# Performance work log

Measured on AMD Instinct MI355X. Metric: run time of the kernel, lower is better.

The kernel has to match this reference:

```python
import jax, jax.numpy as jnp
import numpy as np

B, S, H = 1, 2048, 1024          # batch, seq, hidden_size
INTER, K, DST, DTR = 2048, 4, 16, 64  # intermediate, kernel, ssm_state, dt_rank


def setup_inputs() -> dict:
    key = jax.random.key(0)
    ks = jax.random.split(key, 10)
    sc = 0.02
    return {
        "x": jax.random.normal(ks[0], (B, S, H), jnp.float32),
        "W_in": jax.random.normal(ks[1], (H, 2 * INTER), jnp.float32) * sc,
        "conv_w": jax.random.normal(ks[2], (K, 1, INTER), jnp.float32) * sc,
        "conv_b": jax.random.normal(ks[3], (INTER,), jnp.float32) * sc,
        "W_x": jax.random.normal(ks[4], (INTER, DTR + 2 * DST), jnp.float32) * sc,
        "W_dt": jax.random.normal(ks[5], (DTR, INTER), jnp.float32) * sc,
        "b_dt": jax.random.normal(ks[6], (INTER,), jnp.float32) * sc,
        "A_log": jax.random.normal(ks[7], (INTER, DST), jnp.float32) * sc,
        "D": jax.random.normal(ks[8], (INTER,), jnp.float32) * sc,
        "W_out": jax.random.normal(ks[9], (INTER, H), jnp.float32) * sc,
    }


def _ssm(dA, dBu, C):
    # dA, dBu: (b, s, h, d); C: (b, s, d) -> y: (b, s, h)
    xs = (jnp.moveaxis(dA, 1, 0), jnp.moveaxis(dBu, 1, 0), jnp.moveaxis(C, 1, 0))
    state0 = jnp.zeros(dA.shape[:1] + dA.shape[2:], dA.dtype)  # (b, h, d)

    def step(state, inp):
        Ai, dBui, Ci = inp  # (b,h,d), (b,h,d), (b,d)
        state = Ai * state + dBui
        y = jnp.einsum('bhd,bd->bh', state, Ci)
        return state, y

    _, ys = jax.lax.scan(step, state0, xs)  # ys: (s, b, h)
    return jnp.moveaxis(ys, 0, 1)


def reference(x, W_in, conv_w, conv_b, W_x, W_dt, b_dt, A_log, D, W_out):
    proj = x @ W_in                              # (b, s, 2*inter)
    raw, gate = jnp.split(proj, 2, axis=-1)      # each (b, s, inter)

    # causal depthwise conv over time, groups = inter
    conv = jax.lax.conv_general_dilated(
        raw, conv_w, window_strides=(1,), padding=[(K - 1, 0)],
        dimension_numbers=('NWC', 'WIO', 'NWC'), feature_group_count=INTER)
    h = jax.nn.silu(conv + conv_b)               # (b, s, inter)

    ssm_p = h @ W_x                              # (b, s, dtr + 2*d)
    ts, Bmat, C = jnp.split(ssm_p, [DTR, DTR + DST], axis=-1)
    dt = jax.nn.softplus(ts @ W_dt + b_dt)       # (b, s, inter)

    A = -jnp.exp(A_log)                          # (inter, d)
    dA = jnp.exp(dt[..., None] * A)              # (b, s, inter, d)
    dBu = dt[..., None] * Bmat[:, :, None, :] * h[..., None]  # (b, s, inter, d)

    y = _ssm(dA, dBu, C)                         # (b, s, inter)
    y = y + h * D
    y = y * jax.nn.silu(gate)
    return y @ W_out                             # (b, s, hidden)
```

## Files before the change

kernel.cpp:

```cpp
#include <hip/hip_runtime.h>
#include <math.h>

#define SEQ   2048
#define HID   1024
#define INTER 2048
#define DST   16
#define DTR   64
#define NP    96
#define NC    128
#define LCH   16
#define KS    16

typedef _Float16 f16;
typedef _Float16 f16x8 __attribute__((ext_vector_type(8)));
typedef _Float16 f16x4v __attribute__((ext_vector_type(4)));
typedef float f32x4 __attribute__((ext_vector_type(4)));

__device__ __forceinline__ float sigmoidf_(float x) { return 1.0f / (1.0f + expf(-x)); }
__device__ __forceinline__ float siluf_(float x)    { return x * sigmoidf_(x); }
__device__ __forceinline__ float softplusf_(float x){ return (x > 20.0f) ? x : log1pf(expf(x)); }

__device__ __forceinline__ int xcd_swz(int bid, int nwg)
{
    int cpx = nwg >> 3;
    return (bid & 7) * cpx + (bid >> 3);
}

__device__ __forceinline__ void tile_transpose(const float* __restrict__ W,
                                               f16* __restrict__ Wt,
                                               int K, int N, int bx, int by, int tid)
{
    __shared__ float t[32][33];
    const int n0 = bx * 32, k0 = by * 32;
    const int j = tid & 31, i0 = tid >> 5;
#pragma unroll
    for (int r = 0; r < 4; ++r)
        t[i0 + r * 8][j] = W[(size_t)(k0 + i0 + r * 8) * N + n0 + j];
    __syncthreads();
#pragma unroll
    for (int r = 0; r < 4; ++r)
        Wt[(size_t)(n0 + i0 + r * 8) * K + k0 + j] = (f16)t[j][i0 + r * 8];
}

__global__ __launch_bounds__(256) void prep_all(const float* __restrict__ x,
                                                const float* __restrict__ W_in,
                                                const float* __restrict__ W_out,
                                                const float* __restrict__ W_x,
                                                const float* __restrict__ W_dt,
                                                f16* __restrict__ xh,
                                                f16* __restrict__ W_in_t,
                                                f16* __restrict__ W_out_t,
                                                f16* __restrict__ WxT,
                                                f16* __restrict__ WdtT)
{
    const int bid = blockIdx.x, tid = threadIdx.x;
    if (bid < 2048) {
        int i = (bid * 256 + tid) * 4;
        float4 v = *(const float4*)&x[i];
        f16x4v o;
        o.x = (f16)v.x; o.y = (f16)v.y; o.z = (f16)v.z; o.w = (f16)v.w;
        *(f16x4v*)&xh[i] = o;
    } else if (bid < 6144) {
        int t = bid - 2048;
        tile_transpose(W_in, W_in_t, HID, 4096, t & 127, t >> 7, tid);
    } else if (bid < 8192) {
        int t = bid - 6144;
        tile_transpose(W_out, W_out_t, INTER, HID, t & 31, t >> 5, tid);
    } else if (bid < 8384) {
        int t = bid - 8192;
        tile_transpose(W_x, WxT, INTER, NP, t % 3, t / 3, tid);
    } else {
        int t = bid - 8384;
        tile_transpose(W_dt, WdtT, DTR, INTER, t & 63, t >> 6, tid);
    }
}

template<int BM, int BN, int KK, typename OutT>
__global__ __launch_bounds__(256) void gemm_f16mfma(const f16* __restrict__ Ah,
                                                    const f16* __restrict__ Bt,
                                                    OutT* __restrict__ C,
                                                    int N, int nbx)
{
    constexpr int BK = 64;
    __shared__ __align__(16) f16 As[BM * BK];
    __shared__ __align__(16) f16 Bs[BN * BK];

    const int tile = xcd_swz(blockIdx.x, gridDim.x);
    const int bx = tile % nbx, by = tile / nbx;

    const int tid = threadIdx.x;
    const int wid = tid >> 6, lane = tid & 63;
    const int wr = wid >> 1, wc = wid & 1;
    const int m0 = by * BM, n0 = bx * BN;
    const int l15 = lane & 15, lhi = lane >> 4;

    constexpr int MR = BM / 32;
    constexpr int NR = BN / 32;

    f32x4 acc[MR][NR] = {};

    for (int k0 = 0; k0 < KK; k0 += BK) {
        constexpr int CA = BM * BK * 2 / 1024;
#pragma unroll
        for (int c0 = 0; c0 < CA; c0 += 4) {
            int c = c0 + wid;
            int e = c * 64 + lane;
            int row = e >> 3, seg = e & 7;
            __builtin_amdgcn_global_load_lds(
                (const __attribute__((address_space(1))) unsigned int*)
                    (Ah + (size_t)(m0 + row) * KK + k0 + seg * 8),
                (__attribute__((address_space(3))) unsigned int*)(As + c * 512),
                16, 0, 0);
        }
        constexpr int CB = BN * BK * 2 / 1024;
#pragma unroll
        for (int c0 = 0; c0 < CB; c0 += 4) {
            int c = c0 + wid;
            int e = c * 64 + lane;
            int row = e >> 3, seg = e & 7;
            __builtin_amdgcn_global_load_lds(
                (const __attribute__((address_space(1))) unsigned int*)
                    (Bt + (size_t)(n0 + row) * KK + k0 + seg * 8),
                (__attribute__((address_space(3))) unsigned int*)(Bs + c * 512),
                16, 0, 0);
        }
        __syncthreads();

#pragma unroll
        for (int kk = 0; kk < BK; kk += 32) {
            f16x8 af[MR], bf[NR];
#pragma unroll
            for (int i = 0; i < MR; ++i)
                af[i] = *(const f16x8*)&As[(wr * (BM / 2) + i * 16 + l15) * BK + kk + lhi * 8];
#pragma unroll
            for (int n = 0; n < NR; ++n)
                bf[n] = *(const f16x8*)&Bs[(wc * (BN / 2) + n * 16 + l15) * BK + kk + lhi * 8];
#pragma unroll
            for (int i = 0; i < MR; ++i)
#pragma unroll
                for (int n = 0; n < NR; ++n)
                    acc[i][n] = __builtin_amdgcn_mfma_f32_16x16x32_f16(af[i], bf[n], acc[i][n], 0, 0, 0);
        }
        __syncthreads();
    }

#pragma unroll
    for (int i = 0; i < MR; ++i)
#pragma unroll
        for (int n = 0; n < NR; ++n)
#pragma unroll
            for (int r = 0; r < 4; ++r)
                C[(size_t)(m0 + wr * (BM / 2) + i * 16 + lhi * 4 + r) * N
                  + n0 + wc * (BN / 2) + n * 16 + l15] = (OutT)acc[i][n][r];
}

__global__ __launch_bounds__(256) void hwx_mfma(const f16* __restrict__ hh,
                                                const f16* __restrict__ WxT,
                                                f16* __restrict__ partials)
{
    constexpr int BM = 128, BN = 96, BK = 64;
    __shared__ __align__(16) f16 As[BM * BK];
    __shared__ __align__(16) f16 Bs[BN * BK];

    const int tile = xcd_swz(blockIdx.x, gridDim.x);
    const int bxm = tile & 15, ks = tile >> 4;

    const int tid = threadIdx.x;
    const int wid = tid >> 6, lane = tid & 63;
    const int wr = wid >> 1, wc = wid & 1;
    const int m0 = bxm * BM;
    const int l15 = lane & 15, lhi = lane >> 4;

    constexpr int MR = 4, NR = 3;
    f32x4 acc[MR][NR] = {};

    for (int k0 = ks * 128; k0 < ks * 128 + 128; k0 += BK) {
#pragma unroll
        for (int c0 = 0; c0 < 16; c0 += 4) {
            int c = c0 + wid;
            int e = c * 64 + lane;
            int row = e >> 3, seg = e & 7;
            __builtin_amdgcn_global_load_lds(
                (const __attribute__((address_space(1))) unsigned int*)
                    (hh + (size_t)(m0 + row) * INTER + k0 + seg * 8),
                (__attribute__((address_space(3))) unsigned int*)(As + c * 512),
                16, 0, 0);
        }
#pragma unroll
        for (int c0 = 0; c0 < 12; c0 += 4) {
            int c = c0 + wid;
            int e = c * 64 + lane;
            int row = e >> 3, seg = e & 7;
            __builtin_amdgcn_global_load_lds(
                (const __attribute__((address_space(1))) unsigned int*)
                    (WxT + (size_t)row * INTER + k0 + seg * 8),
                (__attribute__((address_space(3))) unsigned int*)(Bs + c * 512),
                16, 0, 0);
        }
        __syncthreads();

#pragma unroll
        for (int kk = 0; kk < BK; kk += 32) {
            f16x8 af[MR], bf[NR];
#pragma unroll
            for (int i = 0; i < MR; ++i)
                af[i] = *(const f16x8*)&As[(wr * 64 + i * 16 + l15) * BK + kk + lhi * 8];
#pragma unroll
            for (int n = 0; n < NR; ++n)
                bf[n] = *(const f16x8*)&Bs[(wc * 48 + n * 16 + l15) * BK + kk + lhi * 8];
#pragma unroll
            for (int i = 0; i < MR; ++i)
#pragma unroll
                for (int n = 0; n < NR; ++n)
                    acc[i][n] = __builtin_amdgcn_mfma_f32_16x16x32_f16(af[i], bf[n], acc[i][n], 0, 0, 0);
        }
        __syncthreads();
    }

    f16* P = partials + (size_t)ks * (SEQ * NP);
#pragma unroll
    for (int i = 0; i < MR; ++i)
#pragma unroll
        for (int n = 0; n < NR; ++n)
#pragma unroll
            for (int r = 0; r < 4; ++r)
                P[(size_t)(m0 + wr * 64 + i * 16 + lhi * 4 + r) * NP
                  + wc * 48 + n * 16 + l15] = (f16)acc[i][n][r];
}

__global__ __launch_bounds__(256) void reduce_partials(const f16* __restrict__ partials,
                                                       float* __restrict__ ssm_p,
                                                       f16* __restrict__ tsh)
{
    int t = blockIdx.x * 256 + threadIdx.x;
    int i8 = t * 8;
    int s = i8 / NP, j0 = i8 % NP;
    float a[8] = {};
#pragma unroll
    for (int c = 0; c < KS; ++c) {
        f16x8 v = *(const f16x8*)&partials[(size_t)c * (SEQ * NP) + i8];
#pragma unroll
        for (int j = 0; j < 8; ++j) a[j] += (float)v[j];
    }
    if (j0 < DTR) {
        f16x8 o;
#pragma unroll
        for (int j = 0; j < 8; ++j) o[j] = (f16)a[j];
        *(f16x8*)&tsh[(size_t)s * DTR + j0] = o;
    } else {
        *(float4*)&ssm_p[(size_t)s * NP + j0]     = make_float4(a[0], a[1], a[2], a[3]);
        *(float4*)&ssm_p[(size_t)s * NP + j0 + 4] = make_float4(a[4], a[5], a[6], a[7]);
    }
}

__global__ __launch_bounds__(256) void dt_mfma(const f16* __restrict__ tsh,
                                               const f16* __restrict__ WdtT,
                                               const float* __restrict__ bdt,
                                               f16* __restrict__ dtbh)
{
    constexpr int BM = 128, BN = 128, BK = 64;
    __shared__ __align__(16) f16 As[BM * BK];
    __shared__ __align__(16) f16 Bs[BN * BK];

    const int tile = xcd_swz(blockIdx.x, gridDim.x);
    const int bx = tile & 15, by = tile >> 4;

    const int tid = threadIdx.x;
    const int wid = tid >> 6, lane = tid & 63;
    const int wr = wid >> 1, wc = wid & 1;
    const int m0 = by * BM, n0 = bx * BN;
    const int l15 = lane & 15, lhi = lane >> 4;

    constexpr int MR = 4, NR = 4;
    f32x4 acc[MR][NR] = {};

#pragma unroll
    for (int c0 = 0; c0 < 16; c0 += 4) {
        int c = c0 + wid;
        int e = c * 64 + lane;
        int row = e >> 3, seg = e & 7;
        __builtin_amdgcn_global_load_lds(
            (const __attribute__((address_space(1))) unsigned int*)
                (tsh + (size_t)(m0 + row) * DTR + seg * 8),
            (__attribute__((address_space(3))) unsigned int*)(As + c * 512),
            16, 0, 0);
        __builtin_amdgcn_global_load_lds(
            (const __attribute__((address_space(1))) unsigned int*)
                (WdtT + (size_t)(n0 + row) * DTR + seg * 8),
            (__attribute__((address_space(3))) unsigned int*)(Bs + c * 512),
            16, 0, 0);
    }
    __syncthreads();

#pragma unroll
    for (int kk = 0; kk < 64; kk += 32) {
        f16x8 af[MR], bf[NR];
#pragma unroll
        for (int i = 0; i < MR; ++i)
            af[i] = *(const f16x8*)&As[(wr * 64 + i * 16 + l15) * BK + kk + lhi * 8];
#pragma unroll
        for (int n = 0; n < NR; ++n)
            bf[n] = *(const f16x8*)&Bs[(wc * 64 + n * 16 + l15) * BK + kk + lhi * 8];
#pragma unroll
        for (int i = 0; i < MR; ++i)
#pragma unroll
            for (int n = 0; n < NR; ++n)
                acc[i][n] = __builtin_amdgcn_mfma_f32_16x16x32_f16(af[i], bf[n], acc[i][n], 0, 0, 0);
    }

#pragma unroll
    for (int i = 0; i < MR; ++i)
#pragma unroll
        for (int n = 0; n < NR; ++n) {
            int col = n0 + wc * 64 + n * 16 + l15;
            float bv = bdt[col];
#pragma unroll
            for (int r = 0; r < 4; ++r)
                dtbh[(size_t)(m0 + wr * 64 + i * 16 + lhi * 4 + r) * INTER + col] =
                    (f16)softplusf_(acc[i][n][r] + bv);
        }
}

__global__ __launch_bounds__(256) void conv_silu(const f16* __restrict__ projh,
                                                 const float* __restrict__ cw,
                                                 const float* __restrict__ cb,
                                                 f16* __restrict__ hh)
{
    int idx = blockIdx.x * 256 + threadIdx.x;
    int c8 = (idx & (INTER / 8 - 1)) * 8;
    int s = idx >> 8;
    float acc[8];
#pragma unroll
    for (int j = 0; j < 8; ++j) acc[j] = cb[c8 + j];
#pragma unroll
    for (int k = 0; k < 4; ++k) {
        int sp = s + k - 3;
        if (sp >= 0) {
            f16x8 p = *(const f16x8*)&projh[(size_t)sp * (2 * INTER) + c8];
#pragma unroll
            for (int j = 0; j < 8; ++j)
                acc[j] = fmaf((float)p[j], cw[k * INTER + c8 + j], acc[j]);
        }
    }
    f16x8 o;
#pragma unroll
    for (int j = 0; j < 8; ++j) o[j] = (f16)siluf_(acc[j]);
    *(f16x8*)&hh[(size_t)idx * 8] = o;
}

__global__ __launch_bounds__(256) void ssm_pass1(const f16* __restrict__ dtbh,
                                                 const f16* __restrict__ hh,
                                                 const float* __restrict__ ssm_p,
                                                 const float* __restrict__ A_log,
                                                 float* __restrict__ Sbuf,
                                                 float* __restrict__ Pbuf)
{
    const int h = blockIdx.x * 256 + threadIdx.x;
    const int c = blockIdx.y;
    const int s0 = c * LCH;

    __shared__ float Bs[LCH][DST];
    for (int j = threadIdx.x; j < LCH * DST; j += 256) {
        int r = j >> 4, dd = j & 15;
        Bs[r][dd] = ssm_p[(size_t)(s0 + r) * NP + DTR + dd];
    }
    __syncthreads();

    float A[DST], st[DST];
#pragma unroll
    for (int d = 0; d < DST; ++d) {
        A[d] = -__expf(A_log[(size_t)h * DST + d]);
        st[d] = 0.0f;
    }

    float dtsum = 0.0f;
    for (int r = 0; r < LCH; ++r) {
        float dtv = (float)dtbh[(size_t)(s0 + r) * INTER + h];
        float hv  = (float)hh[(size_t)(s0 + r) * INTER + h];
        float dh = dtv * hv;
        dtsum += dtv;
#pragma unroll
        for (int d = 0; d < DST; ++d) {
            float da = __expf(dtv * A[d]);
            st[d] = fmaf(da, st[d], dh * Bs[r][d]);
        }
    }

    size_t base = ((size_t)c * INTER + h) * DST;
#pragma unroll
    for (int d = 0; d < DST; d += 4) {
        *(float4*)&Sbuf[base + d] = make_float4(st[d], st[d+1], st[d+2], st[d+3]);
        float4 p4;
        p4.x = __expf(A[d]     * dtsum);
        p4.y = __expf(A[d + 1] * dtsum);
        p4.z = __expf(A[d + 2] * dtsum);
        p4.w = __expf(A[d + 3] * dtsum);
        *(float4*)&Pbuf[base + d] = p4;
    }
}

__global__ __launch_bounds__(256) void ssm_pass2(const float* __restrict__ Sbuf,
                                                 const float* __restrict__ Pbuf,
                                                 float* __restrict__ Cin)
{
    int i = blockIdx.x * 256 + threadIdx.x;
    float carry = 0.0f;
#pragma unroll 8
    for (int c = 0; c < NC; ++c) {
        size_t idx = (size_t)c * (INTER * DST) + i;
        Cin[idx] = carry;
        carry = fmaf(Pbuf[idx], carry, Sbuf[idx]);
    }
}

__global__ __launch_bounds__(256) void ssm_pass3(const f16* __restrict__ dtbh,
                                                 const f16* __restrict__ hh,
                                                 const float* __restrict__ ssm_p,
                                                 const f16* __restrict__ projh,
                                                 const float* __restrict__ A_log,
                                                 const float* __restrict__ Dvec,
                                                 const float* __restrict__ Cin,
                                                 f16* __restrict__ yh)
{
    const int h = blockIdx.x * 256 + threadIdx.x;
    const int c = blockIdx.y;
    const int s0 = c * LCH;

    __shared__ float Bs[LCH][DST];
    __shared__ float Cs[LCH][DST];
    for (int j = threadIdx.x; j < LCH * DST; j += 256) {
        int r = j >> 4, dd = j & 15;
        Bs[r][dd] = ssm_p[(size_t)(s0 + r) * NP + DTR + dd];
        Cs[r][dd] = ssm_p[(size_t)(s0 + r) * NP + DTR + DST + dd];
    }
    __syncthreads();

    float A[DST], st[DST];
    size_t base = ((size_t)c * INTER + h) * DST;
#pragma unroll
    for (int d = 0; d < DST; ++d) {
        A[d] = -__expf(A_log[(size_t)h * DST + d]);
        st[d] = Cin[base + d];
    }
    const float Dv = Dvec[h];

    for (int r = 0; r < LCH; ++r) {
        float dtv = (float)dtbh[(size_t)(s0 + r) * INTER + h];
        float hv  = (float)hh[(size_t)(s0 + r) * INTER + h];
        float g   = (float)projh[(size_t)(s0 + r) * (2 * INTER) + INTER + h];
        float dh = dtv * hv;
        float y = 0.0f;
#pragma unroll
        for (int d = 0; d < DST; ++d) {
            float da = __expf(dtv * A[d]);
            st[d] = fmaf(da, st[d], dh * Bs[r][d]);
            y = fmaf(st[d], Cs[r][d], y);
        }
        y = fmaf(hv, Dv, y);
        yh[(size_t)(s0 + r) * INTER + h] = (f16)(y * siluf_(g));
    }
}

extern "C" void kernel_launch(void* const* d_in, const int* in_sizes, int n_in,
                              void* d_out, int out_size, void* d_ws, size_t ws_size,
                              hipStream_t stream)
{
    const float* x      = (const float*)d_in[0];
    const float* W_in   = (const float*)d_in[1];
    const float* conv_w = (const float*)d_in[2];
    const float* conv_b = (const float*)d_in[3];
    const float* W_x    = (const float*)d_in[4];
    const float* W_dt   = (const float*)d_in[5];
    const float* b_dt   = (const float*)d_in[6];
    const float* A_log  = (const float*)d_in[7];
    const float* Dv     = (const float*)d_in[8];
    const float* W_out  = (const float*)d_in[9];
    float* out = (float*)d_out;

    float* ws = (float*)d_ws;
    f16*  projh  = (f16*)ws;
    f16*  hh     = (f16*)(ws + 4194304);
    f16*  dtbh   = (f16*)(ws + 6291456);
    f16*  yh     = (f16*)(ws + 8388608);
    f16*  xh     = (f16*)(ws + 10485760);
    f16*  W_in_t = (f16*)(ws + 11534336);
    f16*  W_out_t= (f16*)(ws + 13631488);
    f16*  WxT    = (f16*)(ws + 14680064);
    f16*  tsh    = (f16*)(ws + 14778368);
    f16*  WdtT   = (f16*)(ws + 14843904);
    float* ssm_p = ws + 14909440;
    f16*  parts  = (f16*)(ws + 15106048);
    float* Sbuf  = ws + 16678912;
    float* Pbuf  = ws + 20873216;
    float* Cin   = ws + 25067520;

    prep_all<<<8512, 256, 0, stream>>>(x, W_in, W_out, W_x, W_dt,
                                       xh, W_in_t, W_out_t, WxT, WdtT);

    gemm_f16mfma<128, 128, HID, f16><<<512, 256, 0, stream>>>(
        xh, W_in_t, projh, 2 * INTER, 32);

    conv_silu<<<(SEQ * INTER / 8) / 256, 256, 0, stream>>>(projh, conv_w, conv_b, hh);

    hwx_mfma<<<256, 256, 0, stream>>>(hh, WxT, parts);
    reduce_partials<<<(SEQ * NP / 8) / 256, 256, 0, stream>>>(parts, ssm_p, tsh);

    dt_mfma<<<256, 256, 0, stream>>>(tsh, WdtT, b_dt, dtbh);

    ssm_pass1<<<dim3(INTER / 256, NC), 256, 0, stream>>>(dtbh, hh, ssm_p, A_log, Sbuf, Pbuf);
    ssm_pass2<<<(INTER * DST) / 256, 256, 0, stream>>>(Sbuf, Pbuf, Cin);
    ssm_pass3<<<dim3(INTER / 256, NC), 256, 0, stream>>>(dtbh, hh, ssm_p, projh, A_log, Dv, Cin, yh);

    gemm_f16mfma<64, 128, INTER, float><<<256, 256, 0, stream>>>(
        yh, W_out_t, out, HID, 8);
}
```

Baseline: 183.0 us.

## Fuse all stages into one cooperative persistent kernel with grid syncs

Replaces the ten separate kernel launches with a single cooperative persistent kernel that loops over each phase's work items and separates phases with grid-wide syncs, falling back to per-phase kernels if cooperative launch is unavailable. It also changes the SSM chunking from 128 chunks of 16 steps to 64 chunks of 32 steps. The aim is to remove launch overhead and inter-kernel gaps. In exchange it adds grid-sync costs, caps occupancy at the cooperative grid size (at most 512 blocks, 2 per CU), and drops the XCD-aware tile swizzle.

```diff
diff --git a/kernel.cpp b/kernel.cpp
--- a/kernel.cpp
+++ b/kernel.cpp
@@ -1,5 +1,8 @@
 #include <hip/hip_runtime.h>
+#include <hip/hip_cooperative_groups.h>
 #include <math.h>
+
+namespace cg = cooperative_groups;
 
 #define SEQ   2048
 #define HID   1024
@@ -7,8 +10,8 @@
 #define DST   16
 #define DTR   64
 #define NP    96
-#define NC    128
-#define LCH   16
+#define NC    64
+#define LCH   32
 #define KS    16
 
 typedef _Float16 f16;
@@ -20,86 +23,73 @@
 __device__ __forceinline__ float siluf_(float x)    { return x * sigmoidf_(x); }
 __device__ __forceinline__ float softplusf_(float x){ return (x > 20.0f) ? x : log1pf(expf(x)); }
 
-__device__ __forceinline__ int xcd_swz(int bid, int nwg)
-{
-    int cpx = nwg >> 3;
-    return (bid & 7) * cpx + (bid >> 3);
-}
+struct MegaArgs {
+    const float* x; const float* W_in; const float* W_out; const float* W_x; const float* W_dt;
+    const float* conv_w; const float* conv_b; const float* b_dt; const float* A_log; const float* Dv;
+    float* out;
+    f16* xh; f16* W_in_t; f16* W_out_t; f16* WxT; f16* WdtT;
+    f16* projh; f16* hh; f16* dtbh; f16* yh; f16* tsh; f16* parts;
+    float* ssm_p; float* Sbuf; float* Pbuf; float* Cin;
+};
 
 __device__ __forceinline__ void tile_transpose(const float* __restrict__ W,
                                                f16* __restrict__ Wt,
-                                               int K, int N, int bx, int by, int tid)
-{
-    __shared__ float t[32][33];
+                                               int K, int N, int bx, int by,
+                                               int tid, float* t)
+{
     const int n0 = bx * 32, k0 = by * 32;
     const int j = tid & 31, i0 = tid >> 5;
+    __syncthreads();
 #pragma unroll
     for (int r = 0; r < 4; ++r)
-        t[i0 + r * 8][j] = W[(size_t)(k0 + i0 + r * 8) * N + n0 + j];
+        t[(i0 + r * 8) * 33 + j] = W[(size_t)(k0 + i0 + r * 8) * N + n0 + j];
     __syncthreads();
 #pragma unroll
     for (int r = 0; r < 4; ++r)
-        Wt[(size_t)(n0 + i0 + r * 8) * K + k0 + j] = (f16)t[j][i0 + r * 8];
-}
-
-__global__ __launch_bounds__(256) void prep_all(const float* __restrict__ x,
-                                                const float* __restrict__ W_in,
-                                                const float* __restrict__ W_out,
-                                                const float* __restrict__ W_x,
-                                                const float* __restrict__ W_dt,
-                                                f16* __restrict__ xh,
-                                                f16* __restrict__ W_in_t,
-                                                f16* __restrict__ W_out_t,
-                                                f16* __restrict__ WxT,
-                                                f16* __restrict__ WdtT)
-{
-    const int bid = blockIdx.x, tid = threadIdx.x;
-    if (bid < 2048) {
-        int i = (bid * 256 + tid) * 4;
-        float4 v = *(const float4*)&x[i];
+        Wt[(size_t)(n0 + i0 + r * 8) * K + k0 + j] = (f16)t[j * 33 + i0 + r * 8];
+}
+
+__device__ __forceinline__ void phase_prep(const MegaArgs& a, int v, int tid, float* t)
+{
+    if (v < 2048) {
+        int i = (v * 256 + tid) * 4;
+        float4 w = *(const float4*)&a.x[i];
         f16x4v o;
-        o.x = (f16)v.x; o.y = (f16)v.y; o.z = (f16)v.z; o.w = (f16)v.w;
-        *(f16x4v*)&xh[i] = o;
-    } else if (bid < 6144) {
-        int t = bid - 2048;
-        tile_transpose(W_in, W_in_t, HID, 4096, t & 127, t >> 7, tid);
-    } else if (bid < 8192) {
-        int t = bid - 6144;
-        tile_transpose(W_out, W_out_t, INTER, HID, t & 31, t >> 5, tid);
-    } else if (bid < 8384) {
-        int t = bid - 8192;
-        tile_transpose(W_x, WxT, INTER, NP, t % 3, t / 3, tid);
+        o.x = (f16)w.x; o.y = (f16)w.y; o.z = (f16)w.z; o.w = (f16)w.w;
+        *(f16x4v*)&a.xh[i] = o;
+    } else if (v < 6144) {
+        int q = v - 2048;
+        tile_transpose(a.W_in, a.W_in_t, HID, 4096, q & 127, q >> 7, tid, t);
+    } else if (v < 8192) {
+        int q = v - 6144;
+        tile_transpose(a.W_out, a.W_out_t, INTER, HID, q & 31, q >> 5, tid, t);
+    } else if (v < 8384) {
+        int q = v - 8192;
+        tile_transpose(a.W_x, a.WxT, INTER, NP, q % 3, q / 3, tid, t);
     } else {
-        int t = bid - 8384;
-        tile_transpose(W_dt, WdtT, DTR, INTER, t & 63, t >> 6, tid);
-    }
-}
-
-template<int BM, int BN, int KK, typename OutT>
-__global__ __launch_bounds__(256) void gemm_f16mfma(const f16* __restrict__ Ah,
-                                                    const f16* __restrict__ Bt,
-                                                    OutT* __restrict__ C,
-                                                    int N, int nbx)
+        int q = v - 8384;
+        tile_transpose(a.W_dt, a.WdtT, DTR, INTER, q & 63, q >> 6, tid, t);
+    }
+}
+
+template<int BM, int BN, int KTOT, typename OutT>
+__device__ __forceinline__ void gemm_tile(const f16* __restrict__ Ah,
+                                          const f16* __restrict__ Bt,
+                                          OutT* __restrict__ C, int N,
+                                          int bx, int by, int tid,
+                                          f16* As, f16* Bs)
 {
     constexpr int BK = 64;
-    __shared__ __align__(16) f16 As[BM * BK];
-    __shared__ __align__(16) f16 Bs[BN * BK];
-
-    const int tile = xcd_swz(blockIdx.x, gridDim.x);
-    const int bx = tile % nbx, by = tile / nbx;
-
-    const int tid = threadIdx.x;
     const int wid = tid >> 6, lane = tid & 63;
     const int wr = wid >> 1, wc = wid & 1;
     const int m0 = by * BM, n0 = bx * BN;
     const int l15 = lane & 15, lhi = lane >> 4;
-
     constexpr int MR = BM / 32;
     constexpr int NR = BN / 32;
 
     f32x4 acc[MR][NR] = {};
 
-    for (int k0 = 0; k0 < KK; k0 += BK) {
+    for (int k0 = 0; k0 < KTOT; k0 += BK) {
         constexpr int CA = BM * BK * 2 / 1024;
 #pragma unroll
         for (int c0 = 0; c0 < CA; c0 += 4) {
@@ -108,7 +98,7 @@
             int row = e >> 3, seg = e & 7;
             __builtin_amdgcn_global_load_lds(
                 (const __attribute__((address_space(1))) unsigned int*)
-                    (Ah + (size_t)(m0 + row) * KK + k0 + seg * 8),
+                    (Ah + (size_t)(m0 + row) * KTOT + k0 + seg * 8),
                 (__attribute__((address_space(3))) unsigned int*)(As + c * 512),
                 16, 0, 0);
         }
@@ -120,7 +110,7 @@
             int row = e >> 3, seg = e & 7;
             __builtin_amdgcn_global_load_lds(
                 (const __attribute__((address_space(1))) unsigned int*)
-                    (Bt + (size_t)(n0 + row) * KK + k0 + seg * 8),
+                    (Bt + (size_t)(n0 + row) * KTOT + k0 + seg * 8),
                 (__attribute__((address_space(3))) unsigned int*)(Bs + c * 512),
                 16, 0, 0);
         }
@@ -154,25 +144,40 @@
                   + n0 + wc * (BN / 2) + n * 16 + l15] = (OutT)acc[i][n][r];
 }
 
-__global__ __launch_bounds__(256) void hwx_mfma(const f16* __restrict__ hh,
-                                                const f16* __restrict__ WxT,
-                                                f16* __restrict__ partials)
+__device__ __forceinline__ void phase_conv(const MegaArgs& a, int v, int tid)
+{
+    int idx = v * 256 + tid;
+    int col = (idx & (INTER / 8 - 1)) * 8;
+    int s = idx >> 8;
+    float acc[8];
+#pragma unroll
+    for (int j = 0; j < 8; ++j) acc[j] = a.conv_b[col + j];
+#pragma unroll
+    for (int k = 0; k < 4; ++k) {
+        int sp = s + k - 3;
+        if (sp >= 0) {
+            f16x8 p = *(const f16x8*)&a.projh[(size_t)sp * 4096 + col];
+#pragma unroll
+            for (int j = 0; j < 8; ++j)
+                acc[j] = fmaf((float)p[j], a.conv_w[k * INTER + col + j], acc[j]);
+        }
+    }
+    f16x8 o;
+#pragma unroll
+    for (int j = 0; j < 8; ++j) o[j] = (f16)siluf_(acc[j]);
+    *(f16x8*)&a.hh[(size_t)s * INTER + col] = o;
+}
+
+__device__ __forceinline__ void phase_hwx(const MegaArgs& a, int v, int tid,
+                                          f16* As, f16* Bs)
 {
     constexpr int BM = 128, BN = 96, BK = 64;
-    __shared__ __align__(16) f16 As[BM * BK];
-    __shared__ __align__(16) f16 Bs[BN * BK];
-
-    const int tile = xcd_swz(blockIdx.x, gridDim.x);
-    const int bxm = tile & 15, ks = tile >> 4;
-
-    const int tid = threadIdx.x;
+    const int bxm = v & 15, ks = v >> 4;
     const int wid = tid >> 6, lane = tid & 63;
     const int wr = wid >> 1, wc = wid & 1;
     const int m0 = bxm * BM;
     const int l15 = lane & 15, lhi = lane >> 4;
-
-    constexpr int MR = 4, NR = 3;
-    f32x4 acc[MR][NR] = {};
+    f32x4 acc[4][3] = {};
 
     for (int k0 = ks * 128; k0 < ks * 128 + 128; k0 += BK) {
 #pragma unroll
@@ -182,7 +187,7 @@
             int row = e >> 3, seg = e & 7;
             __builtin_amdgcn_global_load_lds(
                 (const __attribute__((address_space(1))) unsigned int*)
-                    (hh + (size_t)(m0 + row) * INTER + k0 + seg * 8),
+                    (a.hh + (size_t)(m0 + row) * INTER + k0 + seg * 8),
                 (__attribute__((address_space(3))) unsigned int*)(As + c * 512),
                 16, 0, 0);
         }
@@ -193,7 +198,7 @@
             int row = e >> 3, seg = e & 7;
             __builtin_amdgcn_global_load_lds(
                 (const __attribute__((address_space(1))) unsigned int*)
-                    (WxT + (size_t)row * INTER + k0 + seg * 8),
+                    (a.WxT + (size_t)row * INTER + k0 + seg * 8),
                 (__attribute__((address_space(3))) unsigned int*)(Bs + c * 512),
                 16, 0, 0);
         }
@@ -201,78 +206,65 @@
 
 #pragma unroll
         for (int kk = 0; kk < BK; kk += 32) {
-            f16x8 af[MR], bf[NR];
-#pragma unroll
-            for (int i = 0; i < MR; ++i)
+            f16x8 af[4], bf[3];
+#pragma unroll
+            for (int i = 0; i < 4; ++i)
                 af[i] = *(const f16x8*)&As[(wr * 64 + i * 16 + l15) * BK + kk + lhi * 8];
 #pragma unroll
-            for (int n = 0; n < NR; ++n)
+            for (int n = 0; n < 3; ++n)
                 bf[n] = *(const f16x8*)&Bs[(wc * 48 + n * 16 + l15) * BK + kk + lhi * 8];
 #pragma unroll
-            for (int i = 0; i < MR; ++i)
-#pragma unroll
-                for (int n = 0; n < NR; ++n)
+            for (int i = 0; i < 4; ++i)
+#pragma unroll
+                for (int n = 0; n < 3; ++n)
                     acc[i][n] = __builtin_amdgcn_mfma_f32_16x16x32_f16(af[i], bf[n], acc[i][n], 0, 0, 0);
         }
         __syncthreads();
     }
 
-    f16* P = partials + (size_t)ks * (SEQ * NP);
-#pragma unroll
-    for (int i = 0; i < MR; ++i)
-#pragma unroll
-        for (int n = 0; n < NR; ++n)
+    f16* P = a.parts + (size_t)ks * (SEQ * NP);
+#pragma unroll
+    for (int i = 0; i < 4; ++i)
+#pragma unroll
+        for (int n = 0; n < 3; ++n)
 #pragma unroll
             for (int r = 0; r < 4; ++r)
                 P[(size_t)(m0 + wr * 64 + i * 16 + lhi * 4 + r) * NP
                   + wc * 48 + n * 16 + l15] = (f16)acc[i][n][r];
 }
 
-__global__ __launch_bounds__(256) void reduce_partials(const f16* __restrict__ partials,
-                                                       float* __restrict__ ssm_p,
-                                                       f16* __restrict__ tsh)
-{
-    int t = blockIdx.x * 256 + threadIdx.x;
-    int i8 = t * 8;
+__device__ __forceinline__ void phase_reduce(const MegaArgs& a, int v, int tid)
+{
+    int i8 = (v * 256 + tid) * 8;
     int s = i8 / NP, j0 = i8 % NP;
-    float a[8] = {};
+    float acc[8] = {};
 #pragma unroll
     for (int c = 0; c < KS; ++c) {
-        f16x8 v = *(const f16x8*)&partials[(size_t)c * (SEQ * NP) + i8];
-#pragma unroll
-        for (int j = 0; j < 8; ++j) a[j] += (float)v[j];
+        f16x8 w = *(const f16x8*)&a.parts[(size_t)c * (SEQ * NP) + i8];
+#pragma unroll
+        for (int j = 0; j < 8; ++j) acc[j] += (float)w[j];
     }
     if (j0 < DTR) {
         f16x8 o;
 #pragma unroll
-        for (int j = 0; j < 8; ++j) o[j] = (f16)a[j];
-        *(f16x8*)&tsh[(size_t)s * DTR + j0] = o;
+        for (int j = 0; j < 8; ++j) o[j] = (f16)acc[j];
+        *(f16x8*)&a.tsh[(size_t)s * DTR + j0] = o;
     } else {
-        *(float4*)&ssm_p[(size_t)s * NP + j0]     = make_float4(a[0], a[1], a[2], a[3]);
-        *(float4*)&ssm_p[(size_t)s * NP + j0 + 4] = make_float4(a[4], a[5], a[6], a[7]);
-    }
-}
-
-__global__ __launch_bounds__(256) void dt_mfma(const f16* __restrict__ tsh,
-                                               const f16* __restrict__ WdtT,
-                                               const float* __restrict__ bdt,
-                                               f16* __restrict__ dtbh)
-{
-    constexpr int BM = 128, BN = 128, BK = 64;
-    __shared__ __align__(16) f16 As[BM * BK];
-    __shared__ __align__(16) f16 Bs[BN * BK];
-
-    const int tile = xcd_swz(blockIdx.x, gridDim.x);
-    const int bx = tile & 15, by = tile >> 4;
-
-    const int tid = threadIdx.x;
+        *(float4*)&a.ssm_p[(size_t)s * NP + j0]     = make_float4(acc[0], acc[1], acc[2], acc[3]);
+        *(float4*)&a.ssm_p[(size_t)s * NP + j0 + 4] = make_float4(acc[4], acc[5], acc[6], acc[7]);
+    }
+}
+
+__device__ __forceinline__ void phase_dt(const MegaArgs& a, int v, int tid,
+                                         f16* As, f16* Bs)
+{
+    constexpr int BK = 64;
+    const int bx = v & 15, by = v >> 4;
     const int wid = tid >> 6, lane = tid & 63;
     const int wr = wid >> 1, wc = wid & 1;
-    const int m0 = by * BM, n0 = bx * BN;
+    const int m0 = by * 128, n0 = bx * 128;
     const int l15 = lane & 15, lhi = lane >> 4;
-
-    constexpr int MR = 4, NR = 4;
-    f32x4 acc[MR][NR] = {};
+    f32x4 acc[4][4] = {};
 
 #pragma unroll
     for (int c0 = 0; c0 < 16; c0 += 4) {
@@ -281,12 +273,12 @@
         int row = e >> 3, seg = e & 7;
         __builtin_amdgcn_global_load_lds(
             (const __attribute__((address_space(1))) unsigned int*)
-                (tsh + (size_t)(m0 + row) * DTR + seg * 8),
+                (a.tsh + (size_t)(m0 + row) * DTR + seg * 8),
             (__attribute__((address_space(3))) unsigned int*)(As + c * 512),
             16, 0, 0);
         __builtin_amdgcn_global_load_lds(
             (const __attribute__((address_space(1))) unsigned int*)
-                (WdtT + (size_t)(n0 + row) * DTR + seg * 8),
+                (a.WdtT + (size_t)(n0 + row) * DTR + seg * 8),
             (__attribute__((address_space(3))) unsigned int*)(Bs + c * 512),
             16, 0, 0);
     }
@@ -294,144 +286,99 @@
 
 #pragma unroll
     for (int kk = 0; kk < 64; kk += 32) {
-        f16x8 af[MR], bf[NR];
-#pragma unroll
-        for (int i = 0; i < MR; ++i)
+        f16x8 af[4], bf[4];
+#pragma unroll
+        for (int i = 0; i < 4; ++i)
             af[i] = *(const f16x8*)&As[(wr * 64 + i * 16 + l15) * BK + kk + lhi * 8];
 #pragma unroll
-        for (int n = 0; n < NR; ++n)
+        for (int n = 0; n < 4; ++n)
             bf[n] = *(const f16x8*)&Bs[(wc * 64 + n * 16 + l15) * BK + kk + lhi * 8];
 #pragma unroll
-        for (int i = 0; i < MR; ++i)
-#pragma unroll
-            for (int n = 0; n < NR; ++n)
+        for (int i = 0; i < 4; ++i)
+#pragma unroll
+            for (int n = 0; n < 4; ++n)
                 acc[i][n] = __builtin_amdgcn_mfma_f32_16x16x32_f16(af[i], bf[n], acc[i][n], 0, 0, 0);
     }
 
 #pragma unroll
-    for (int i = 0; i < MR; ++i)
-#pragma unroll
-        for (int n = 0; n < NR; ++n) {
+    for (int i = 0; i < 4; ++i)
+#pragma unroll
+        for (int n = 0; n < 4; ++n) {
             int col = n0 + wc * 64 + n * 16 + l15;
-            float bv = bdt[col];
+            float bv = a.b_dt[col];
 #pragma unroll
             for (int r = 0; r < 4; ++r)
-                dtbh[(size_t)(m0 + wr * 64 + i * 16 + lhi * 4 + r) * INTER + col] =
+                a.dtbh[(size_t)(m0 + wr * 64 + i * 16 + lhi * 4 + r) * INTER + col] =
                     (f16)softplusf_(acc[i][n][r] + bv);
         }
-}
-
-__global__ __launch_bounds__(256) void conv_silu(const f16* __restrict__ projh,
-                                                 const float* __restrict__ cw,
-                                                 const float* __restrict__ cb,
-                                                 f16* __restrict__ hh)
-{
-    int idx = blockIdx.x * 256 + threadIdx.x;
-    int c8 = (idx & (INTER / 8 - 1)) * 8;
-    int s = idx >> 8;
-    float acc[8];
-#pragma unroll
-    for (int j = 0; j < 8; ++j) acc[j] = cb[c8 + j];
-#pragma unroll
-    for (int k = 0; k < 4; ++k) {
-        int sp = s + k - 3;
-        if (sp >= 0) {
-            f16x8 p = *(const f16x8*)&projh[(size_t)sp * (2 * INTER) + c8];
-#pragma unroll
-            for (int j = 0; j < 8; ++j)
-                acc[j] = fmaf((float)p[j], cw[k * INTER + c8 + j], acc[j]);
-        }
-    }
-    f16x8 o;
-#pragma unroll
-    for (int j = 0; j < 8; ++j) o[j] = (f16)siluf_(acc[j]);
-    *(f16x8*)&hh[(size_t)idx * 8] = o;
-}
-
-__global__ __launch_bounds__(256) void ssm_pass1(const f16* __restrict__ dtbh,
-                                                 const f16* __restrict__ hh,
-                                                 const float* __restrict__ ssm_p,
-                                                 const float* __restrict__ A_log,
-                                                 float* __restrict__ Sbuf,
-                                                 float* __restrict__ Pbuf)
-{
-    const int h = blockIdx.x * 256 + threadIdx.x;
-    const int c = blockIdx.y;
+    __syncthreads();
+}
+
+__device__ __forceinline__ void phase_pass1(const MegaArgs& a, int v, int tid, float* Bsc)
+{
+    const int hblk = v >> 6, c = v & 63;
+    const int h = hblk * 256 + tid;
     const int s0 = c * LCH;
-
-    __shared__ float Bs[LCH][DST];
-    for (int j = threadIdx.x; j < LCH * DST; j += 256) {
+    for (int j = tid; j < LCH * DST; j += 256) {
         int r = j >> 4, dd = j & 15;
-        Bs[r][dd] = ssm_p[(size_t)(s0 + r) * NP + DTR + dd];
+        Bsc[r * DST + dd] = a.ssm_p[(size_t)(s0 + r) * NP + DTR + dd];
     }
     __syncthreads();
 
     float A[DST], st[DST];
 #pragma unroll
     for (int d = 0; d < DST; ++d) {
-        A[d] = -__expf(A_log[(size_t)h * DST + d]);
+        A[d] = -__expf(a.A_log[(size_t)h * DST + d]);
         st[d] = 0.0f;
     }
-
     float dtsum = 0.0f;
     for (int r = 0; r < LCH; ++r) {
-        float dtv = (float)dtbh[(size_t)(s0 + r) * INTER + h];
-        float hv  = (float)hh[(size_t)(s0 + r) * INTER + h];
+        float dtv = (float)a.dtbh[(size_t)(s0 + r) * INTER + h];
+        float hv  = (float)a.hh[(size_t)(s0 + r) * INTER + h];
         float dh = dtv * hv;
         dtsum += dtv;
 #pragma unroll
         for (int d = 0; d < DST; ++d) {
             float da = __expf(dtv * A[d]);
-            st[d] = fmaf(da, st[d], dh * Bs[r][d]);
-        }
-    }
-
+            st[d] = fmaf(da, st[d], dh * Bsc[r * DST + d]);
+        }
+    }
     size_t base = ((size_t)c * INTER + h) * DST;
 #pragma unroll
     for (int d = 0; d < DST; d += 4) {
-        *(float4*)&Sbuf[base + d] = make_float4(st[d], st[d+1], st[d+2], st[d+3]);
+        *(float4*)&a.Sbuf[base + d] = make_float4(st[d], st[d+1], st[d+2], st[d+3]);
         float4 p4;
         p4.x = __expf(A[d]     * dtsum);
         p4.y = __expf(A[d + 1] * dtsum);
         p4.z = __expf(A[d + 2] * dtsum);
         p4.w = __expf(A[d + 3] * dtsum);
-        *(float4*)&Pbuf[base + d] = p4;
-    }
-}
-
-__global__ __launch_bounds__(256) void ssm_pass2(const float* __restrict__ Sbuf,
-                                                 const float* __restrict__ Pbuf,
-                                                 float* __restrict__ Cin)
-{
-    int i = blockIdx.x * 256 + threadIdx.x;
+        *(float4*)&a.Pbuf[base + d] = p4;
+    }
+    __syncthreads();
+}
+
+__device__ __forceinline__ void phase_pass2(const MegaArgs& a, int v, int tid)
+{
+    int i = v * 256 + tid;
     float carry = 0.0f;
 #pragma unroll 8
     for (int c = 0; c < NC; ++c) {
         size_t idx = (size_t)c * (INTER * DST) + i;
-        Cin[idx] = carry;
-        carry = fmaf(Pbuf[idx], carry, Sbuf[idx]);
-    }
-}
-
-__global__ __launch_bounds__(256) void ssm_pass3(const f16* __restrict__ dtbh,
-                                                 const f16* __restrict__ hh,
-                                                 const float* __restrict__ ssm_p,
-                                                 const f16* __restrict__ projh,
-                                                 const float* __restrict__ A_log,
-                                                 const float* __restrict__ Dvec,
-                                                 const float* __restrict__ Cin,
-                                                 f16* __restrict__ yh)
-{
-    const int h = blockIdx.x * 256 + threadIdx.x;
-    const int c = blockIdx.y;
+        a.Cin[idx] = carry;
+        carry = fmaf(a.Pbuf[idx], carry, a.Sbuf[idx]);
+    }
+}
+
+__device__ __forceinline__ void phase_pass3(const MegaArgs& a, int v, int tid, float* Bsc)
+{
+    float* Csc = Bsc + LCH * DST;
+    const int hblk = v >> 6, c = v & 63;
+    const int h = hblk * 256 + tid;
     const int s0 = c * LCH;
-
-    __shared__ float Bs[LCH][DST];
-    __shared__ float Cs[LCH][DST];
-    for (int j = threadIdx.x; j < LCH * DST; j += 256) {
+    for (int j = tid; j < LCH * DST; j += 256) {
         int r = j >> 4, dd = j & 15;
-        Bs[r][dd] = ssm_p[(size_t)(s0 + r) * NP + DTR + dd];
-        Cs[r][dd] = ssm_p[(size_t)(s0 + r) * NP + DTR + DST + dd];
+        Bsc[r * DST + dd] = a.ssm_p[(size_t)(s0 + r) * NP + DTR + dd];
+        Csc[r * DST + dd] = a.ssm_p[(size_t)(s0 + r) * NP + DTR + DST + dd];
     }
     __syncthreads();
 
@@ -439,78 +386,186 @@
     size_t base = ((size_t)c * INTER + h) * DST;
 #pragma unroll
     for (int d = 0; d < DST; ++d) {
-        A[d] = -__expf(A_log[(size_t)h * DST + d]);
-        st[d] = Cin[base + d];
-    }
-    const float Dv = Dvec[h];
+        A[d] = -__expf(a.A_log[(size_t)h * DST + d]);
+        st[d] = a.Cin[base + d];
+    }
+    const float Dvv = a.Dv[h];
 
     for (int r = 0; r < LCH; ++r) {
-        float dtv = (float)dtbh[(size_t)(s0 + r) * INTER + h];
-        float hv  = (float)hh[(size_t)(s0 + r) * INTER + h];
-        float g   = (float)projh[(size_t)(s0 + r) * (2 * INTER) + INTER + h];
+        float dtv = (float)a.dtbh[(size_t)(s0 + r) * INTER + h];
+        float hv  = (float)a.hh[(size_t)(s0 + r) * INTER + h];
+        float g   = (float)a.projh[(size_t)(s0 + r) * 4096 + INTER + h];
         float dh = dtv * hv;
         float y = 0.0f;
 #pragma unroll
         for (int d = 0; d < DST; ++d) {
             float da = __expf(dtv * A[d]);
-            st[d] = fmaf(da, st[d], dh * Bs[r][d]);
-            y = fmaf(st[d], Cs[r][d], y);
-        }
-        y = fmaf(hv, Dv, y);
-        yh[(size_t)(s0 + r) * INTER + h] = (f16)(y * siluf_(g));
-    }
+            st[d] = fmaf(da, st[d], dh * Bsc[r * DST + d]);
+            y = fmaf(st[d], Csc[r * DST + d], y);
+        }
+        y = fmaf(hv, Dvv, y);
+        a.yh[(size_t)(s0 + r) * INTER + h] = (f16)(y * siluf_(g));
+    }
+    __syncthreads();
+}
+
+__global__ __launch_bounds__(256, 2) void mega(MegaArgs a)
+{
+    cg::grid_group grid = cg::this_grid();
+    const int bid = blockIdx.x, tid = threadIdx.x;
+    const int G = gridDim.x;
+    __shared__ __align__(16) unsigned char smem[32768];
+
+    for (int v = bid; v < 8512; v += G) phase_prep(a, v, tid, (float*)smem);
+    grid.sync();
+    for (int v = bid; v < 512; v += G)
+        gemm_tile<128, 128, HID, f16>(a.xh, a.W_in_t, a.projh, 4096,
+                                      v % 32, v / 32, tid,
+                                      (f16*)smem, (f16*)(smem + 16384));
+    grid.sync();
+    for (int v = bid; v < 2048; v += G) phase_conv(a, v, tid);
+    grid.sync();
+    for (int v = bid; v < 256; v += G)
+        phase_hwx(a, v, tid, (f16*)smem, (f16*)(smem + 16384));
+    grid.sync();
+    for (int v = bid; v < 96; v += G) phase_reduce(a, v, tid);
+    grid.sync();
+    for (int v = bid; v < 256; v += G)
+        phase_dt(a, v, tid, (f16*)smem, (f16*)(smem + 16384));
+    grid.sync();
+    for (int v = bid; v < 512; v += G) phase_pass1(a, v, tid, (float*)smem);
+    grid.sync();
+    for (int v = bid; v < 128; v += G) phase_pass2(a, v, tid);
+    grid.sync();
+    for (int v = bid; v < 512; v += G) phase_pass3(a, v, tid, (float*)smem);
+    grid.sync();
+    for (int v = bid; v < 256; v += G)
+        gemm_tile<64, 128, INTER, float>(a.yh, a.W_out_t, a.out, HID,
+                                         v & 7, v >> 3, tid,
+                                         (f16*)smem, (f16*)(smem + 8192));
+}
+
+__global__ __launch_bounds__(256) void k_prep(MegaArgs a)
+{
+    __shared__ float t[32 * 33];
+    phase_prep(a, blockIdx.x, threadIdx.x, t);
+}
+__global__ __launch_bounds__(256) void k_gemm1(MegaArgs a)
+{
+    __shared__ __align__(16) f16 As[128 * 64];
+    __shared__ __align__(16) f16 Bs[128 * 64];
+    gemm_tile<128, 128, HID, f16>(a.xh, a.W_in_t, a.projh, 4096,
+                                  (int)blockIdx.x % 32, (int)blockIdx.x / 32,
+                                  threadIdx.x, As, Bs);
+}
+__global__ __launch_bounds__(256) void k_conv(MegaArgs a)
+{
+    phase_conv(a, blockIdx.x, threadIdx.x);
+}
+__global__ __launch_bounds__(256) void k_hwx(MegaArgs a)
+{
+    __shared__ __align__(16) f16 As[128 * 64];
+    __shared__ __align__(16) f16 Bs[96 * 64];
+    phase_hwx(a, blockIdx.x, threadIdx.x, As, Bs);
+}
+__global__ __launch_bounds__(256) void k_reduce(MegaArgs a)
+{
+    phase_reduce(a, blockIdx.x, threadIdx.x);
+}
+__global__ __launch_bounds__(256) void k_dt(MegaArgs a)
+{
+    __shared__ __align__(16) f16 As[128 * 64];
+    __shared__ __align__(16) f16 Bs[128 * 64];
+    phase_dt(a, blockIdx.x, threadIdx.x, As, Bs);
+}
+__global__ __launch_bounds__(256) void k_pass1(MegaArgs a)
+{
+    __shared__ float b[LCH * DST];
+    phase_pass1(a, blockIdx.x, threadIdx.x, b);
+}
+__global__ __launch_bounds__(256) void k_pass2(MegaArgs a)
+{
+    phase_pass2(a, blockIdx.x, threadIdx.x);
+}
+__global__ __launch_bounds__(256) void k_pass3(MegaArgs a)
+{
+    __shared__ float b[2 * LCH * DST];
+    phase_pass3(a, blockIdx.x, threadIdx.x, b);
+}
+__global__ __launch_bounds__(256) void k_gemm2(MegaArgs a)
+{
+    __shared__ __align__(16) f16 As[64 * 64];
+    __shared__ __align__(16) f16 Bs[128 * 64];
+    gemm_tile<64, 128, INTER, float>(a.yh, a.W_out_t, a.out, HID,
+                                     (int)blockIdx.x & 7, (int)blockIdx.x >> 3,
+                                     threadIdx.x, As, Bs);
 }
 
 extern "C" void kernel_launch(void* const* d_in, const int* in_sizes, int n_in,
                               void* d_out, int out_size, void* d_ws, size_t ws_size,
                               hipStream_t stream)
 {
-    const float* x      = (const float*)d_in[0];
-    const float* W_in   = (const float*)d_in[1];
-    const float* conv_w = (const float*)d_in[2];
-    const float* conv_b = (const float*)d_in[3];
-    const float* W_x    = (const float*)d_in[4];
-    const float* W_dt   = (const float*)d_in[5];
-    const float* b_dt   = (const float*)d_in[6];
-    const float* A_log  = (const float*)d_in[7];
-    const float* Dv     = (const float*)d_in[8];
-    const float* W_out  = (const float*)d_in[9];
-    float* out = (float*)d_out;
-
     float* ws = (float*)d_ws;
-    f16*  projh  = (f16*)ws;
-    f16*  hh     = (f16*)(ws + 4194304);
-    f16*  dtbh   = (f16*)(ws + 6291456);
-    f16*  yh     = (f16*)(ws + 8388608);
-    f16*  xh     = (f16*)(ws + 10485760);
-    f16*  W_in_t = (f16*)(ws + 11534336);
-    f16*  W_out_t= (f16*)(ws + 13631488);
-    f16*  WxT    = (f16*)(ws + 14680064);
-    f16*  tsh    = (f16*)(ws + 14778368);
-    f16*  WdtT   = (f16*)(ws + 14843904);
-    float* ssm_p = ws + 14909440;
-    f16*  parts  = (f16*)(ws + 15106048);
-    float* Sbuf  = ws + 16678912;
-    float* Pbuf  = ws + 20873216;
-    float* Cin   = ws + 25067520;
-
-    prep_all<<<8512, 256, 0, stream>>>(x, W_in, W_out, W_x, W_dt,
-                                       xh, W_in_t, W_out_t, WxT, WdtT);
-
-    gemm_f16mfma<128, 128, HID, f16><<<512, 256, 0, stream>>>(
-        xh, W_in_t, projh, 2 * INTER, 32);
-
-    conv_silu<<<(SEQ * INTER / 8) / 256, 256, 0, stream>>>(projh, conv_w, conv_b, hh);
-
-    hwx_mfma<<<256, 256, 0, stream>>>(hh, WxT, parts);
-    reduce_partials<<<(SEQ * NP / 8) / 256, 256, 0, stream>>>(parts, ssm_p, tsh);
-
-    dt_mfma<<<256, 256, 0, stream>>>(tsh, WdtT, b_dt, dtbh);
-
-    ssm_pass1<<<dim3(INTER / 256, NC), 256, 0, stream>>>(dtbh, hh, ssm_p, A_log, Sbuf, Pbuf);
-    ssm_pass2<<<(INTER * DST) / 256, 256, 0, stream>>>(Sbuf, Pbuf, Cin);
-    ssm_pass3<<<dim3(INTER / 256, NC), 256, 0, stream>>>(dtbh, hh, ssm_p, projh, A_log, Dv, Cin, yh);
-
-    gemm_f16mfma<64, 128, INTER, float><<<256, 256, 0, stream>>>(
-        yh, W_out_t, out, HID, 8);
-}
+    MegaArgs a;
+    a.x      = (const float*)d_in[0];
+    a.W_in   = (const float*)d_in[1];
+    a.conv_w = (const float*)d_in[2];
+    a.conv_b = (const float*)d_in[3];
+    a.W_x    = (const float*)d_in[4];
+    a.W_dt   = (const float*)d_in[5];
+    a.b_dt   = (const float*)d_in[6];
+    a.A_log  = (const float*)d_in[7];
+    a.Dv     = (const float*)d_in[8];
+    a.W_out  = (const float*)d_in[9];
+    a.out    = (float*)d_out;
+
+    a.projh  = (f16*)ws;
+    a.hh     = (f16*)(ws + 4194304);
+    a.dtbh   = (f16*)(ws + 6291456);
+    a.yh     = (f16*)(ws + 8388608);
+    a.xh     = (f16*)(ws + 10485760);
+    a.W_in_t = (f16*)(ws + 11534336);
+    a.W_out_t= (f16*)(ws + 13631488);
+    a.WxT    = (f16*)(ws + 14680064);
+    a.tsh    = (f16*)(ws + 14778368);
+    a.WdtT   = (f16*)(ws + 14843904);
+    a.ssm_p  = ws + 14909440;
+    a.parts  = (f16*)(ws + 15106048);
+    a.Sbuf   = ws + 16678912;
+    a.Pbuf   = ws + 18776064;
+    a.Cin    = ws + 20873216;
+
+    bool coop_ok = false;
+    int dev = 0;
+    if (hipGetDevice(&dev) == hipSuccess) {
+        int attr = 0, ncu = 0, maxb = 0;
+        hipDeviceGetAttribute(&attr, hipDeviceAttributeCooperativeLaunch, dev);
+        hipDeviceGetAttribute(&ncu, hipDeviceAttributeMultiprocessorCount, dev);
+        hipError_t oe = hipOccupancyMaxActiveBlocksPerMultiprocessor(&maxb, mega, 256, 0);
+        if (attr && oe == hipSuccess && maxb > 0 && ncu > 0) {
+            int grid = maxb * ncu;
+            if (grid > 512) grid = 512;
+            if (grid >= 256) {
+                void* params[] = { (void*)&a };
+                hipError_t e = hipLaunchCooperativeKernel((const void*)mega,
+                                                          dim3(grid), dim3(256),
+                                                          params, 0, stream);
+                if (e == hipSuccess) coop_ok = true;
+                else (void)hipGetLastError();
+            }
+        }
+    }
+
+    if (!coop_ok) {
+        k_prep  <<<8512, 256, 0, stream>>>(a);
+        k_gemm1 <<<512,  256, 0, stream>>>(a);
+        k_conv  <<<2048, 256, 0, stream>>>(a);
+        k_hwx   <<<256,  256, 0, stream>>>(a);
+        k_reduce<<<96,   256, 0, stream>>>(a);
+        k_dt    <<<256,  256, 0, stream>>>(a);
+        k_pass1 <<<512,  256, 0, stream>>>(a);
+        k_pass2 <<<128,  256, 0, stream>>>(a);
+        k_pass3 <<<512,  256, 0, stream>>>(a);
+        k_gemm2 <<<256,  256, 0, stream>>>(a);
+    }
+}
```

After: 514.5 us. +181.1%, slower.
